# Optimization experiments

Hardware: AMD Instinct MI355X
Metric: run time of the kernel (lower is better)

Reference implementation:

```python
import jax, jax.numpy as jnp
import numpy as np

D_MODEL = 1024
N_HEADS = 16
D_K = D_MODEL // N_HEADS
ROPE_THETA = 10000.0


def setup_inputs() -> dict:
    key = jax.random.key(0)
    ks = jax.random.split(key, 5)
    B, S = 2, 2048
    scale = 1.0 / np.sqrt(D_MODEL)
    return {
        "x": jax.random.normal(ks[0], (B, S, D_MODEL), dtype=jnp.float32),
        "token_positions": jnp.arange(S, dtype=jnp.int32),
        "Wq": jax.random.normal(ks[1], (D_MODEL, D_MODEL), dtype=jnp.float32) * scale,
        "Wk": jax.random.normal(ks[2], (D_MODEL, D_MODEL), dtype=jnp.float32) * scale,
        "Wv": jax.random.normal(ks[3], (D_MODEL, D_MODEL), dtype=jnp.float32) * scale,
        "Wo": jax.random.normal(ks[4], (D_MODEL, D_MODEL), dtype=jnp.float32) * scale,
    }


def apply_rope(x, positions):
    # x: [b, h, s, d_k]; interleaved-pair rotary embedding, theta=10000
    half = D_K // 2
    inv_freq = ROPE_THETA ** (-jnp.arange(0, half, dtype=x.dtype) * 2.0 / D_K)  # [half]
    angles = positions.astype(x.dtype)[:, None] * inv_freq[None, :]             # [s, half]
    cos, sin = jnp.cos(angles), jnp.sin(angles)                                 # [s, half]
    x1 = x[..., 0::2]
    x2 = x[..., 1::2]
    r1 = x1 * cos - x2 * sin
    r2 = x1 * sin + x2 * cos
    # re-interleave
    return jnp.stack([r1, r2], axis=-1).reshape(x.shape)


def reference(x, token_positions, Wq, Wk, Wv, Wo):
    B, S, _ = x.shape
    # Linear(d_model, d_model) with no bias: y = x @ W.T
    Q = jnp.einsum("bsd,ed->bse", x, Wq).reshape(B, S, N_HEADS, D_K).transpose(0, 2, 1, 3)
    K = jnp.einsum("bsd,ed->bse", x, Wk).reshape(B, S, N_HEADS, D_K).transpose(0, 2, 1, 3)
    V = jnp.einsum("bsd,ed->bse", x, Wv).reshape(B, S, N_HEADS, D_K).transpose(0, 2, 1, 3)
    Q = apply_rope(Q, token_positions)
    K = apply_rope(K, token_positions)
    scores = jnp.einsum("bhqd,bhkd->bhqk", Q, K) / jnp.sqrt(jnp.asarray(D_K, x.dtype))
    causal = jnp.tril(jnp.ones((S, S), dtype=bool))
    scores = jnp.where(causal[None, None, :, :], scores, jnp.asarray(-jnp.inf, x.dtype))
    attn = jax.nn.softmax(scores, axis=-1)
    out = jnp.einsum("bhqk,bhkd->bhqd", attn, V)            # [b, h, s, d_k]
    out = out.transpose(0, 2, 1, 3).reshape(B, S, D_MODEL)   # [b, s, d_model]
    return jnp.einsum("bsd,ed->bse", out, Wo)
```

## Files before the change

### kernel.cpp

```cpp
#include <hip/hip_runtime.h>
#include <math.h>

#define SEQ 2048
#define NH  16
#define DKH 64
#define DM  1024
#define MR  4096

using bf16x8 = __attribute__((ext_vector_type(8))) short;
using f32x4  = __attribute__((ext_vector_type(4))) float;

__device__ __forceinline__ ushort f2b(float f) {
  unsigned u = __float_as_uint(f);
  return (ushort)((u + 0x7fffu + ((u >> 16) & 1u)) >> 16);
}

__device__ __forceinline__ void gll16(const void* g, void* l) {
  __builtin_amdgcn_global_load_lds(
      (const __attribute__((address_space(1))) void*)g,
      (__attribute__((address_space(3))) void*)l, 16, 0, 0);
}

__global__ __launch_bounds__(256) void cvt_all(
    const float* __restrict__ x,  const float* __restrict__ wq,
    const float* __restrict__ wk, const float* __restrict__ wv,
    const float* __restrict__ wo,
    ushort* __restrict__ xb,  ushort* __restrict__ wqb, ushort* __restrict__ wkb,
    ushort* __restrict__ wvb, ushort* __restrict__ wob)
{
  size_t e = ((size_t)blockIdx.x * 256 + threadIdx.x) * 4;
  const float* s; ushort* d; size_t off;
  if      (e < 4194304) { s = x;  d = xb;  off = e; }
  else if (e < 5242880) { s = wq; d = wqb; off = e - 4194304; }
  else if (e < 6291456) { s = wk; d = wkb; off = e - 5242880; }
  else if (e < 7340032) { s = wv; d = wvb; off = e - 6291456; }
  else                  { s = wo; d = wob; off = e - 7340032; }
  float4 f = *(const float4*)(s + off);
  ushort4 o4 = { f2b(f.x), f2b(f.y), f2b(f.z), f2b(f.w) };
  *(ushort4*)(d + off) = o4;
}

__global__ __launch_bounds__(256) void gemm_qkv(
    const ushort* __restrict__ X,
    const ushort* __restrict__ Wq, const ushort* __restrict__ Wk, const ushort* __restrict__ Wv,
    ushort* __restrict__ Q, ushort* __restrict__ K, ushort* __restrict__ Vt,
    const int* __restrict__ pos)
{
  __shared__ __align__(16) char smem[32768];
  char* As = smem;
  char* Bs = smem + 16384;

  const int z = blockIdx.z;
  const ushort* W = (z == 0) ? Wq : (z == 1) ? Wk : Wv;

  const int n0 = blockIdx.x * 128;
  const int m0 = blockIdx.y * 128;
  const int tid  = threadIdx.x;
  const int lane = tid & 63;
  const int w    = tid >> 6;
  const int wm = (w >> 1) * 64;
  const int wn = (w & 1) * 64;
  const int li = lane & 15;
  const int g  = lane >> 4;

  f32x4 acc[4][4] = {};

  for (int k0 = 0; k0 < DM; k0 += 64) {
    __syncthreads();
    #pragma unroll
    for (int it = 0; it < 4; ++it) {
      const int L  = w * 4096 + it * 1024 + lane * 16;
      const int r  = L >> 7;
      const int sc = ((L >> 4) & 7) ^ (r & 7);
      gll16(X + (size_t)(m0 + r) * DM + k0 + sc * 8, As + w * 4096 + it * 1024);
      gll16(W + (size_t)(n0 + r) * DM + k0 + sc * 8, Bs + w * 4096 + it * 1024);
    }
    __syncthreads();

    #pragma unroll
    for (int ks = 0; ks < 2; ++ks) {
      bf16x8 af[4], bfr[4];
      #pragma unroll
      for (int mf = 0; mf < 4; ++mf) {
        const int row = wm + mf * 16 + li;
        af[mf] = *(const bf16x8*)(As + row * 128 + (((ks * 4 + g) ^ (row & 7)) << 4));
      }
      #pragma unroll
      for (int nf = 0; nf < 4; ++nf) {
        const int row = wn + nf * 16 + li;
        bfr[nf] = *(const bf16x8*)(Bs + row * 128 + (((ks * 4 + g) ^ (row & 7)) << 4));
      }
      #pragma unroll
      for (int mf = 0; mf < 4; ++mf)
        #pragma unroll
        for (int nf = 0; nf < 4; ++nf)
          acc[mf][nf] = __builtin_amdgcn_mfma_f32_16x16x32_bf16(af[mf], bfr[nf], acc[mf][nf], 0, 0, 0);
    }
  }

  #pragma unroll
  for (int nf = 0; nf < 4; ++nf) {
    const int n = n0 + wn + nf * 16 + li;
    const int h = n >> 6;
    const int d = n & 63;
    if (z == 2) {
      #pragma unroll
      for (int mf = 0; mf < 4; ++mf) {
        const int m  = m0 + wm + mf * 16 + g * 4;
        const int b  = m >> 11;
        const int s2 = m & (SEQ - 1);
        ushort4 pk = { f2b(acc[mf][nf][0]), f2b(acc[mf][nf][1]),
                       f2b(acc[mf][nf][2]), f2b(acc[mf][nf][3]) };
        *(ushort4*)(Vt + (((size_t)b * NH + h) * DKH + d) * SEQ + s2) = pk;
      }
    } else {
      ushort* DST = (z == 0) ? Q : K;
      const float freq = __expf(-(float)(d >> 1) * 0.2878231366242557f);
      #pragma unroll
      for (int mf = 0; mf < 4; ++mf) {
        #pragma unroll
        for (int r = 0; r < 4; ++r) {
          const int m  = m0 + wm + mf * 16 + g * 4 + r;
          const int b  = m >> 11;
          const int s2 = m & (SEQ - 1);
          const float ang = (float)pos[s2] * freq;
          float sn, cs;
          __sincosf(ang, &sn, &cs);
          const float v1 = acc[mf][nf][r];
          const float v2 = __shfl_xor(v1, 1);
          float ov = (d & 1) ? (v2 * sn + v1 * cs)
                             : (v1 * cs - v2 * sn);
          if (z == 0) ov *= 0.125f;
          DST[(((size_t)b * NH + h) * SEQ + s2) * DKH + d] = f2b(ov);
        }
      }
    }
  }
}

__global__ __launch_bounds__(256) void gemm_wo(
    const ushort* __restrict__ A, const ushort* __restrict__ W,
    float* __restrict__ out)
{
  __shared__ __align__(16) char smem[32768];
  char* As = smem;
  char* Bs = smem + 16384;

  const int n0 = blockIdx.x * 128;
  const int m0 = blockIdx.y * 128;
  const int tid  = threadIdx.x;
  const int lane = tid & 63;
  const int w    = tid >> 6;
  const int wm = (w >> 1) * 64;
  const int wn = (w & 1) * 64;
  const int li = lane & 15;
  const int g  = lane >> 4;

  f32x4 acc[4][4] = {};

  for (int k0 = 0; k0 < DM; k0 += 64) {
    __syncthreads();
    #pragma unroll
    for (int it = 0; it < 4; ++it) {
      const int L  = w * 4096 + it * 1024 + lane * 16;
      const int r  = L >> 7;
      const int sc = ((L >> 4) & 7) ^ (r & 7);
      gll16(A + (size_t)(m0 + r) * DM + k0 + sc * 8, As + w * 4096 + it * 1024);
      gll16(W + (size_t)(n0 + r) * DM + k0 + sc * 8, Bs + w * 4096 + it * 1024);
    }
    __syncthreads();

    #pragma unroll
    for (int ks = 0; ks < 2; ++ks) {
      bf16x8 af[4], bfr[4];
      #pragma unroll
      for (int mf = 0; mf < 4; ++mf) {
        const int row = wm + mf * 16 + li;
        af[mf] = *(const bf16x8*)(As + row * 128 + (((ks * 4 + g) ^ (row & 7)) << 4));
      }
      #pragma unroll
      for (int nf = 0; nf < 4; ++nf) {
        const int row = wn + nf * 16 + li;
        bfr[nf] = *(const bf16x8*)(Bs + row * 128 + (((ks * 4 + g) ^ (row & 7)) << 4));
      }
      #pragma unroll
      for (int mf = 0; mf < 4; ++mf)
        #pragma unroll
        for (int nf = 0; nf < 4; ++nf)
          acc[mf][nf] = __builtin_amdgcn_mfma_f32_16x16x32_bf16(af[mf], bfr[nf], acc[mf][nf], 0, 0, 0);
    }
  }

  #pragma unroll
  for (int nf = 0; nf < 4; ++nf)
    #pragma unroll
    for (int mf = 0; mf < 4; ++mf)
      #pragma unroll
      for (int r = 0; r < 4; ++r)
        out[(size_t)(m0 + wm + mf * 16 + g * 4 + r) * DM + n0 + wn + nf * 16 + li] = acc[mf][nf][r];
}

__global__ __launch_bounds__(256) void attn(
    const ushort* __restrict__ Q, const ushort* __restrict__ K,
    const ushort* __restrict__ Vt, ushort* __restrict__ AO)
{
  __shared__ __align__(16) char KsB[2][8192];
  __shared__ __align__(16) char VsB[2][8192];
  __shared__ __align__(16) char Ps[8192];

  const int tid  = threadIdx.x;
  const int lane = tid & 63;
  const int w    = tid >> 6;
  const int li   = lane & 15;
  const int g    = lane >> 4;

  const int bx  = blockIdx.x;
  const int xcd = bx & 7;
  const int idx = bx >> 3;
  const int bh  = (idx & 3) * 8 + xcd;
  const int qb  = 31 - (idx >> 2);
  const int q0b = qb * 64;
  const int n   = qb + 1;
  const int q0w = q0b + w * 16;

  const ushort* Qb = Q  + (size_t)bh * SEQ * DKH;
  const ushort* Kb = K  + (size_t)bh * SEQ * DKH;
  const ushort* Vb = Vt + (size_t)bh * DKH * SEQ;
  char* Pw = Ps + w * 2048;

  const bf16x8 qf0 = *(const bf16x8*)(Qb + (size_t)(q0w + li) * DKH + g * 8);
  const bf16x8 qf1 = *(const bf16x8*)(Qb + (size_t)(q0w + li) * DKH + 32 + g * 8);

  f32x4 o[4] = {};
  float m_ = -INFINITY, l_ = 0.f;

  auto stage = [&](int kt, int buf) {
    const int k0 = kt * 64;
    #pragma unroll
    for (int it = 0; it < 2; ++it) {
      const int L  = w * 2048 + it * 1024 + lane * 16;
      const int r  = L >> 7;
      const int sc = ((L >> 4) & 7) ^ (r & 7);
      gll16(Kb + (size_t)(k0 + r) * DKH + sc * 8, &KsB[buf][w * 2048 + it * 1024]);
      gll16(Vb + (size_t)r * SEQ + k0 + sc * 8,   &VsB[buf][w * 2048 + it * 1024]);
    }
  };

  auto computeT = [&](int t) {
    const int k0 = t * 64;
    const char* Kc = KsB[t & 1];
    const char* Vc = VsB[t & 1];

    f32x4 st[4] = {};
    #pragma unroll
    for (int nf = 0; nf < 4; ++nf) {
      const int row = nf * 16 + li;
      bf16x8 kfa = *(const bf16x8*)(Kc + row * 128 + (((0 + g) ^ (row & 7)) << 4));
      bf16x8 kfb = *(const bf16x8*)(Kc + row * 128 + (((4 + g) ^ (row & 7)) << 4));
      st[nf] = __builtin_amdgcn_mfma_f32_16x16x32_bf16(kfa, qf0, st[nf], 0, 0, 0);
      st[nf] = __builtin_amdgcn_mfma_f32_16x16x32_bf16(kfb, qf1, st[nf], 0, 0, 0);
    }

    #pragma unroll
    for (int nf = 0; nf < 4; ++nf)
      #pragma unroll
      for (int r = 0; r < 4; ++r)
        if (k0 + nf * 16 + g * 4 + r > q0w + li) st[nf][r] = -1e30f;

    float mx = fmaxf(fmaxf(fmaxf(st[0][0], st[0][1]), fmaxf(st[0][2], st[0][3])),
                     fmaxf(fmaxf(st[1][0], st[1][1]), fmaxf(st[1][2], st[1][3])));
    mx = fmaxf(mx, fmaxf(fmaxf(fmaxf(st[2][0], st[2][1]), fmaxf(st[2][2], st[2][3])),
                         fmaxf(fmaxf(st[3][0], st[3][1]), fmaxf(st[3][2], st[3][3]))));
    mx = fmaxf(mx, __shfl_xor(mx, 16));
    mx = fmaxf(mx, __shfl_xor(mx, 32));
    const float newm = fmaxf(m_, mx);
    const float al = __expf(m_ - newm);
    m_ = newm;

    float p[4][4];
    float rs = 0.f;
    #pragma unroll
    for (int nf = 0; nf < 4; ++nf)
      #pragma unroll
      for (int r = 0; r < 4; ++r) {
        p[nf][r] = __expf(st[nf][r] - newm);
        rs += p[nf][r];
      }
    rs += __shfl_xor(rs, 16);
    rs += __shfl_xor(rs, 32);
    l_ = l_ * al + rs;

    float alr[4];
    #pragma unroll
    for (int r = 0; r < 4; ++r) alr[r] = __shfl(al, g * 4 + r);
    #pragma unroll
    for (int nf = 0; nf < 4; ++nf)
      #pragma unroll
      for (int r = 0; r < 4; ++r) o[nf][r] *= alr[r];

    #pragma unroll
    for (int nf = 0; nf < 4; ++nf) {
      ushort4 pk = { f2b(p[nf][0]), f2b(p[nf][1]), f2b(p[nf][2]), f2b(p[nf][3]) };
      const int cw = nf * 2 + (g >> 1);
      *(ushort4*)(Pw + li * 128 + ((cw ^ (li & 7)) << 4) + ((g & 1) << 3)) = pk;
    }
    bf16x8 pf0 = *(const bf16x8*)(Pw + li * 128 + (((0 + g) ^ (li & 7)) << 4));
    bf16x8 pf1 = *(const bf16x8*)(Pw + li * 128 + (((4 + g) ^ (li & 7)) << 4));

    #pragma unroll
    for (int nf = 0; nf < 4; ++nf) {
      const int row = nf * 16 + li;
      bf16x8 vfa = *(const bf16x8*)(Vc + row * 128 + (((0 + g) ^ (row & 7)) << 4));
      bf16x8 vfb = *(const bf16x8*)(Vc + row * 128 + (((4 + g) ^ (row & 7)) << 4));
      o[nf] = __builtin_amdgcn_mfma_f32_16x16x32_bf16(pf0, vfa, o[nf], 0, 0, 0);
      o[nf] = __builtin_amdgcn_mfma_f32_16x16x32_bf16(pf1, vfb, o[nf], 0, 0, 0);
    }
  };

  stage(0, 0);
  for (int t = 0; t < n; ++t) {
    if (t + 1 < n) {
      stage(t + 1, (t + 1) & 1);
      __builtin_amdgcn_sched_barrier(0);
      asm volatile("s_waitcnt vmcnt(4)" ::: "memory");
    } else {
      asm volatile("s_waitcnt vmcnt(0)" ::: "memory");
    }
    __builtin_amdgcn_s_barrier();
    __builtin_amdgcn_sched_barrier(0);
    if (t * 64 <= q0w + 15) computeT(t);
    __builtin_amdgcn_sched_barrier(0);
    __builtin_amdgcn_s_barrier();
  }

  const float inv = 1.0f / l_;
  float ir[4];
  #pragma unroll
  for (int r = 0; r < 4; ++r) ir[r] = __shfl(inv, g * 4 + r);

  const int b = bh >> 4, h = bh & 15;
  #pragma unroll
  for (int nf = 0; nf < 4; ++nf)
    #pragma unroll
    for (int r = 0; r < 4; ++r) {
      const int q = q0w + g * 4 + r;
      AO[((size_t)b * SEQ + q) * DM + h * DKH + nf * 16 + li] = f2b(o[nf][r] * ir[r]);
    }
}

extern "C" void kernel_launch(void* const* d_in, const int* in_sizes, int n_in,
                              void* d_out, int out_size, void* d_ws, size_t ws_size,
                              hipStream_t stream)
{
  const float* x   = (const float*)d_in[0];
  const int*   pos = (const int*)  d_in[1];
  const float* Wq  = (const float*)d_in[2];
  const float* Wk  = (const float*)d_in[3];
  const float* Wv  = (const float*)d_in[4];
  const float* Wo  = (const float*)d_in[5];
  float* out = (float*)d_out;

  ushort* ws  = (ushort*)d_ws;
  ushort* xb  = ws;
  ushort* wqb = xb  + 4194304;
  ushort* wkb = wqb + 1048576;
  ushort* wvb = wkb + 1048576;
  ushort* wob = wvb + 1048576;
  ushort* Qb  = wob + 1048576;
  ushort* Kb  = Qb  + 4194304;
  ushort* Vtb = Kb  + 4194304;
  ushort* AOb = Vtb + 4194304;

  cvt_all<<<8192, 256, 0, stream>>>(x, Wq, Wk, Wv, Wo, xb, wqb, wkb, wvb, wob);
  gemm_qkv<<<dim3(8, 32, 3), 256, 0, stream>>>(xb, wqb, wkb, wvb, Qb, Kb, Vtb, pos);
  attn<<<1024, 256, 0, stream>>>(Qb, Kb, Vtb, AOb);
  gemm_wo<<<dim3(8, 32), 256, 0, stream>>>(AOb, wob, out);
}
```

Measured before the change: 132.2 us.

## Double-buffer LDS tiles in QKV and output projection GEMMs

Both projection GEMMs now use two LDS buffers per operand. The next K-tile is fetched with global_load_lds while the current tile is being multiplied, using explicit vmcnt waits and s_barriers in place of the two __syncthreads per iteration. The aim is to hide global load latency behind the MFMA work. In exchange, LDS use doubles to 64KB per block, which may lower occupancy.

```diff
diff --git a/kernel.cpp b/kernel.cpp
--- a/kernel.cpp
+++ b/kernel.cpp
@@ -46,9 +46,8 @@
     ushort* __restrict__ Q, ushort* __restrict__ K, ushort* __restrict__ Vt,
     const int* __restrict__ pos)
 {
-  __shared__ __align__(16) char smem[32768];
-  char* As = smem;
-  char* Bs = smem + 16384;
+  __shared__ __align__(16) char As[2][16384];
+  __shared__ __align__(16) char Bs[2][16384];
 
   const int z = blockIdx.z;
   const ushort* W = (z == 0) ? Wq : (z == 1) ? Wk : Wv;
@@ -65,30 +64,31 @@
 
   f32x4 acc[4][4] = {};
 
-  for (int k0 = 0; k0 < DM; k0 += 64) {
-    __syncthreads();
+  auto stage = [&](int t, int buf) {
+    const int k0 = t * 64;
     #pragma unroll
     for (int it = 0; it < 4; ++it) {
       const int L  = w * 4096 + it * 1024 + lane * 16;
       const int r  = L >> 7;
       const int sc = ((L >> 4) & 7) ^ (r & 7);
-      gll16(X + (size_t)(m0 + r) * DM + k0 + sc * 8, As + w * 4096 + it * 1024);
-      gll16(W + (size_t)(n0 + r) * DM + k0 + sc * 8, Bs + w * 4096 + it * 1024);
-    }
-    __syncthreads();
-
+      gll16(X + (size_t)(m0 + r) * DM + k0 + sc * 8, &As[buf][w * 4096 + it * 1024]);
+      gll16(W + (size_t)(n0 + r) * DM + k0 + sc * 8, &Bs[buf][w * 4096 + it * 1024]);
+    }
+  };
+
+  auto compute = [&](int buf) {
     #pragma unroll
     for (int ks = 0; ks < 2; ++ks) {
       bf16x8 af[4], bfr[4];
       #pragma unroll
       for (int mf = 0; mf < 4; ++mf) {
         const int row = wm + mf * 16 + li;
-        af[mf] = *(const bf16x8*)(As + row * 128 + (((ks * 4 + g) ^ (row & 7)) << 4));
+        af[mf] = *(const bf16x8*)(&As[buf][row * 128 + (((ks * 4 + g) ^ (row & 7)) << 4)]);
       }
       #pragma unroll
       for (int nf = 0; nf < 4; ++nf) {
         const int row = wn + nf * 16 + li;
-        bfr[nf] = *(const bf16x8*)(Bs + row * 128 + (((ks * 4 + g) ^ (row & 7)) << 4));
+        bfr[nf] = *(const bf16x8*)(&Bs[buf][row * 128 + (((ks * 4 + g) ^ (row & 7)) << 4)]);
       }
       #pragma unroll
       for (int mf = 0; mf < 4; ++mf)
@@ -96,6 +96,22 @@
         for (int nf = 0; nf < 4; ++nf)
           acc[mf][nf] = __builtin_amdgcn_mfma_f32_16x16x32_bf16(af[mf], bfr[nf], acc[mf][nf], 0, 0, 0);
     }
+  };
+
+  stage(0, 0);
+  for (int t = 0; t < 16; ++t) {
+    if (t < 15) {
+      stage(t + 1, (t + 1) & 1);
+      __builtin_amdgcn_sched_barrier(0);
+      asm volatile("s_waitcnt vmcnt(8)" ::: "memory");
+    } else {
+      asm volatile("s_waitcnt vmcnt(0)" ::: "memory");
+    }
+    __builtin_amdgcn_s_barrier();
+    __builtin_amdgcn_sched_barrier(0);
+    compute(t & 1);
+    __builtin_amdgcn_sched_barrier(0);
+    __builtin_amdgcn_s_barrier();
   }
 
   #pragma unroll
@@ -142,9 +158,8 @@
     const ushort* __restrict__ A, const ushort* __restrict__ W,
     float* __restrict__ out)
 {
-  __shared__ __align__(16) char smem[32768];
-  char* As = smem;
-  char* Bs = smem + 16384;
+  __shared__ __align__(16) char As[2][16384];
+  __shared__ __align__(16) char Bs[2][16384];
 
   const int n0 = blockIdx.x * 128;
   const int m0 = blockIdx.y * 128;
@@ -158,30 +173,31 @@
 
   f32x4 acc[4][4] = {};
 
-  for (int k0 = 0; k0 < DM; k0 += 64) {
-    __syncthreads();
+  auto stage = [&](int t, int buf) {
+    const int k0 = t * 64;
     #pragma unroll
     for (int it = 0; it < 4; ++it) {
       const int L  = w * 4096 + it * 1024 + lane * 16;
       const int r  = L >> 7;
       const int sc = ((L >> 4) & 7) ^ (r & 7);
-      gll16(A + (size_t)(m0 + r) * DM + k0 + sc * 8, As + w * 4096 + it * 1024);
-      gll16(W + (size_t)(n0 + r) * DM + k0 + sc * 8, Bs + w * 4096 + it * 1024);
-    }
-    __syncthreads();
-
+      gll16(A + (size_t)(m0 + r) * DM + k0 + sc * 8, &As[buf][w * 4096 + it * 1024]);
+      gll16(W + (size_t)(n0 + r) * DM + k0 + sc * 8, &Bs[buf][w * 4096 + it * 1024]);
+    }
+  };
+
+  auto compute = [&](int buf) {
     #pragma unroll
     for (int ks = 0; ks < 2; ++ks) {
       bf16x8 af[4], bfr[4];
       #pragma unroll
       for (int mf = 0; mf < 4; ++mf) {
         const int row = wm + mf * 16 + li;
-        af[mf] = *(const bf16x8*)(As + row * 128 + (((ks * 4 + g) ^ (row & 7)) << 4));
+        af[mf] = *(const bf16x8*)(&As[buf][row * 128 + (((ks * 4 + g) ^ (row & 7)) << 4)]);
       }
       #pragma unroll
       for (int nf = 0; nf < 4; ++nf) {
         const int row = wn + nf * 16 + li;
-        bfr[nf] = *(const bf16x8*)(Bs + row * 128 + (((ks * 4 + g) ^ (row & 7)) << 4));
+        bfr[nf] = *(const bf16x8*)(&Bs[buf][row * 128 + (((ks * 4 + g) ^ (row & 7)) << 4)]);
       }
       #pragma unroll
       for (int mf = 0; mf < 4; ++mf)
@@ -189,6 +205,22 @@
         for (int nf = 0; nf < 4; ++nf)
           acc[mf][nf] = __builtin_amdgcn_mfma_f32_16x16x32_bf16(af[mf], bfr[nf], acc[mf][nf], 0, 0, 0);
     }
+  };
+
+  stage(0, 0);
+  for (int t = 0; t < 16; ++t) {
+    if (t < 15) {
+      stage(t + 1, (t + 1) & 1);
+      __builtin_amdgcn_sched_barrier(0);
+      asm volatile("s_waitcnt vmcnt(8)" ::: "memory");
+    } else {
+      asm volatile("s_waitcnt vmcnt(0)" ::: "memory");
+    }
+    __builtin_amdgcn_s_barrier();
+    __builtin_amdgcn_sched_barrier(0);
+    compute(t & 1);
+    __builtin_amdgcn_sched_barrier(0);
+    __builtin_amdgcn_s_barrier();
   }
 
   #pragma unroll
```

After: 128.9 us. 1.03x faster.
